# Kernel tuning notes

Hardware: AMD Instinct MI355X
Metric: run time of the kernel (lower is better)

Reference implementation:

```python
import jax, jax.numpy as jnp
import numpy as np

B, N, D = 32, 4096, 256
NC, NTPC, NVPT, NS = 16, 8, 4, 16
NT = NC * NTPC          # 128 type codes
NV = NT * NVPT          # 512 variant codes
THRESH = 0.1            # code_sparsity


def setup_inputs() -> dict:
    key = jax.random.key(0)
    ks = jax.random.split(key, 24)
    rn = lambda k, s, sc=0.02: jax.random.normal(k, s, jnp.float32) * sc
    return {
        "X": jax.random.normal(ks[0], (B, N, D), jnp.float32),
        "positions": jax.random.normal(ks[1], (B, N, D), jnp.float32),
        "mask": jnp.ones((B, N), jnp.bool_),
        "category_codes": rn(ks[2], (NC, D)),
        "type_codes": rn(ks[3], (NT, D)),
        "variant_codes": rn(ks[4], (NV, D)),
        "spatial_codes": rn(ks[5], (NS, D)),
        "log_tau": jnp.zeros((1,), jnp.float32),
        "Wk": rn(ks[6], (D, D)), "bk": jnp.zeros((D,), jnp.float32),
        "Wcat": rn(ks[7], (D, D)), "bcat": jnp.zeros((D,), jnp.float32),
        "Wtype": rn(ks[8], (D, D)), "btype": jnp.zeros((D,), jnp.float32),
        "Wvar": rn(ks[9], (D, D)), "bvar": jnp.zeros((D,), jnp.float32),
        "Wsp": rn(ks[10], (D, D)), "bsp": jnp.zeros((D,), jnp.float32),
        "Wg1": rn(ks[11], (D, 2 * D)), "bg1": jnp.zeros((D,), jnp.float32),
        "Wg2": rn(ks[12], (D, D)), "bg2": jnp.zeros((D,), jnp.float32),
        "Wo": rn(ks[13], (D, D)), "bo": jnp.zeros((D,), jnp.float32),
        "ln_g": jnp.ones((D,), jnp.float32), "ln_b": jnp.zeros((D,), jnp.float32),
        "level_weights": jnp.ones((4,), jnp.float32) / 4.0,
    }


def _sparsify(w, thr):
    w = jnp.where(w > thr, w, 0.0)
    return w / (w.sum(-1, keepdims=True) + 1e-8)


def reference(X, positions, mask, category_codes, type_codes, variant_codes,
              spatial_codes, log_tau, Wk, bk, Wcat, bcat, Wtype, btype,
              Wvar, bvar, Wsp, bsp, Wg1, bg1, Wg2, bg2, Wo, bo, ln_g, ln_b,
              level_weights):
    d = X.shape[-1]
    tau = jnp.clip(jnp.exp(log_tau) + 0.1, 0.1, 2.0)  # (1,)
    mv = jnp.finfo(X.dtype).min / 2
    K = X @ Wk.T + bk  # (B,N,d)

    def level(codes, Wq, bq):
        Q = codes @ Wq.T + bq                                    # (M,d)
        attn = jnp.einsum('md,bnd->bmn', Q, K) / jnp.sqrt(jnp.float32(d))
        attn = jnp.where(mask[:, None, :], attn, mv)
        attn = jnp.clip(attn, -50.0, 50.0)
        G = jnp.nan_to_num(jax.nn.softmax(attn, axis=-1))
        H = jnp.einsum('bmn,bnd->bmd', G, X)                     # (B,M,d)
        w_raw = jnp.linalg.norm(H, axis=-1) / tau                # (B,M)
        return H, w_raw

    # level 0: category
    H_cat, w_cat_raw = level(category_codes, Wcat, bcat)
    w_cat_sparse = _sparsify(jax.nn.softmax(w_cat_raw, -1), THRESH)
    # level 1: type (gated by category)
    H_type, w_type_raw = level(type_codes, Wtype, btype)
    w_type_g = (w_type_raw.reshape(-1, NC, NTPC) * w_cat_sparse[:, :, None]).reshape(-1, NT)
    w_type_sparse = _sparsify(jax.nn.softmax(w_type_g, -1), THRESH / 2)
    # level 2: variant (gated by type)
    H_var, w_var_raw = level(variant_codes, Wvar, bvar)
    w_type_exp = jnp.repeat(w_type_sparse, NVPT, axis=-1)        # (B,NV)
    w_var_sparse = _sparsify(jax.nn.softmax(w_var_raw * w_type_exp, -1), THRESH / 4)
    # spatial (independent)
    H_sp, w_sp_raw = level(spatial_codes, Wsp, bsp)
    w_sp_sparse = _sparsify(jax.nn.softmax(w_sp_raw, -1), THRESH)

    z_cat = jnp.einsum('bm,bmd->bd', w_cat_sparse, H_cat)
    z_type = jnp.einsum('bm,bmd->bd', w_type_sparse, H_type)
    z_var = jnp.einsum('bm,bmd->bd', w_var_sparse, H_var)
    z_sp = jnp.einsum('bm,bmd->bd', w_sp_sparse, H_sp)

    lw = jax.nn.softmax(level_weights)
    z = lw[0] * z_cat + lw[1] * z_type + lw[2] * z_var + lw[3] * z_sp

    # position gate: masked mean-pooled positions -> sigmoid gate
    m = mask.astype(X.dtype)
    pos_pool = (positions * m[:, :, None]).sum(1) / (m.sum(1, keepdims=True) + 1e-8)
    h = jax.nn.gelu(jnp.concatenate([z, pos_pool], -1) @ Wg1.T + bg1, approximate=False)
    gate = jax.nn.sigmoid(h @ Wg2.T + bg2)
    z = z * gate

    # out_proj: Linear + LayerNorm
    y = z @ Wo.T + bo
    mu = y.mean(-1, keepdims=True)
    var = ((y - mu) ** 2).mean(-1, keepdims=True)
    y = (y - mu) / jnp.sqrt(var + 1e-5) * ln_g + ln_b
    return y
```

## Files before the change

kernel.cpp:

```cpp
#include <hip/hip_runtime.h>

typedef unsigned short u16;
typedef short v8s __attribute__((ext_vector_type(8)));
typedef float v4f __attribute__((ext_vector_type(4)));

union U16x8 { uint4 u4; v8s s8; u16 us[8]; };

__device__ __forceinline__ u16 f2bf(float x) {
  unsigned int u = __float_as_uint(x);
  u += 0x7fffu + ((u >> 16) & 1u);
  return (u16)(u >> 16);
}

#define GLOBAL_AS __attribute__((address_space(1)))
#define LDS_AS __attribute__((address_space(3)))
__device__ __forceinline__ void async16(const void* g, void* l) {
  __builtin_amdgcn_global_load_lds((const GLOBAL_AS unsigned int*)g,
                                   (LDS_AS unsigned int*)l, 16, 0, 0);
}

#define BB 32
#define NN 4096
#define DD 256
#define M_TOT 672
#define M_PAD 704
#define MT_PER_B 11
#define NSPLIT 4
#define NCHUNK (NN / NSPLIT)

__global__ void k01_q(const float* __restrict__ cat, const float* __restrict__ typ,
                      const float* __restrict__ var, const float* __restrict__ spc,
                      const float* __restrict__ Wcat, const float* __restrict__ bcat,
                      const float* __restrict__ Wtype, const float* __restrict__ btype,
                      const float* __restrict__ Wvar, const float* __restrict__ bvar,
                      const float* __restrict__ Wsp, const float* __restrict__ bsp,
                      const float* __restrict__ Wk, const float* __restrict__ bk,
                      u16* __restrict__ Qp, float* __restrict__ qbw) {
  __shared__ float cl[DD];
  __shared__ float ql[DD];
  __shared__ float red[4];
  const int m = blockIdx.x, tid = threadIdx.x;
  const float* codes = nullptr; const float* W = nullptr; const float* bia = nullptr; int r = 0;
  if (m < 16)       { codes = cat; r = m;       W = Wcat;  bia = bcat; }
  else if (m < 144) { codes = typ; r = m - 16;  W = Wtype; bia = btype; }
  else if (m < 656) { codes = var; r = m - 144; W = Wvar;  bia = bvar; }
  else if (m < 672) { codes = spc; r = m - 656; W = Wsp;   bia = bsp; }
  cl[tid] = (m < M_TOT) ? codes[r * DD + tid] : 0.f;
  __syncthreads();
  float acc = 0.f;
  if (m < M_TOT) {
    acc = bia[tid];
    const float4* w4 = (const float4*)(W + (size_t)tid * DD);
    const float4* c4 = (const float4*)cl;
    #pragma unroll 8
    for (int k = 0; k < 64; ++k) {
      float4 a = c4[k], b = w4[k];
      acc += a.x * b.x + a.y * b.y + a.z * b.z + a.w * b.w;
    }
  }
  ql[tid] = acc;
  __syncthreads();
  float acc2 = 0.f;
  for (int j = 0; j < DD; ++j) acc2 += ql[j] * Wk[(size_t)j * DD + tid];
  Qp[m * DD + tid] = f2bf(acc2);
  float p = ql[tid] * bk[tid];
  #pragma unroll
  for (int off = 32; off > 0; off >>= 1) p += __shfl_down(p, off, 64);
  if ((tid & 63) == 0) red[tid >> 6] = p;
  __syncthreads();
  if (tid == 0) qbw[m] = red[0] + red[1] + red[2] + red[3];
}

__global__ void k2_cast(const float* __restrict__ X, u16* __restrict__ Xb,
                        u16* __restrict__ XbT) {
  __shared__ u16 tl[64][72];
  const int n0 = blockIdx.x * 64, d0 = blockIdx.y * 64, b = blockIdx.z;
  const int tid = threadIdx.x;
  const int nl = tid >> 4, d4 = tid & 15;
  #pragma unroll
  for (int rr = 0; rr < 4; ++rr) {
    const int n = n0 + nl + rr * 16;
    float4 v = *(const float4*)(X + ((size_t)b * NN + n) * DD + d0 + d4 * 4);
    ushort4 h;
    h.x = f2bf(v.x); h.y = f2bf(v.y); h.z = f2bf(v.z); h.w = f2bf(v.w);
    *(ushort4*)(Xb + ((size_t)b * NN + n) * DD + d0 +
                (((d4 >> 1) ^ (n & 7)) << 3) + (d4 & 1) * 4) = h;
    *(ushort4*)(&tl[nl + rr * 16][d4 * 4]) = h;
  }
  __syncthreads();
  const int dl = tid >> 4, n4 = tid & 15;
  #pragma unroll
  for (int rr = 0; rr < 4; ++rr) {
    const int d = dl + rr * 16;
    ushort4 h;
    h.x = tl[n4 * 4 + 0][d]; h.y = tl[n4 * 4 + 1][d];
    h.z = tl[n4 * 4 + 2][d]; h.w = tl[n4 * 4 + 3][d];
    *(ushort4*)(XbT + ((size_t)b * DD + d0 + d) * NN + n0 +
                (((n4 >> 1) ^ (dl & 7)) << 3) + (n4 & 1) * 4) = h;
  }
}

__global__ __launch_bounds__(256, 2) void pf_fused(
    const u16* __restrict__ Xb, const u16* __restrict__ XbT,
    const u16* __restrict__ Qp, const float* __restrict__ qbw,
    const unsigned char* __restrict__ mask,
    float* __restrict__ HP, float* __restrict__ sumsP) {
  __shared__ u16 sX[64 * 256];
  __shared__ u16 sXT[256 * 64];
  __shared__ u16 sP[64 * 64];

  const int id = blockIdx.x;
  const int xcd = id & 7, lin = id >> 3;
  const int ggl = lin / MT_PER_B, k = lin - ggl * MT_PER_B;
  const int gg = xcd * 16 + ggl;
  const int b = gg >> 2, split = gg & 3;
  const int m0 = k * 64;
  const int ns0 = split * NCHUNK;

  const int tid = threadIdx.x;
  const int lane = tid & 63, w = tid >> 6;
  const int q = lane >> 4, c16 = lane & 15;
  const int wmQ = (w >> 1) * 32, wn = (w & 1) * 32;
  const int wd = w * 64;

  const u16* XbB = Xb + (size_t)b * NN * DD;
  const u16* XTB = XbT + (size_t)b * DD * NN;
  const unsigned char* mkB = mask + (size_t)b * NN;

  auto stageX = [&](int n0g) {
    #pragma unroll
    for (int i = 0; i < 8; ++i) {
      const int c = i * 256 + tid;
      async16(XbB + (size_t)(n0g + (c >> 5)) * DD + (c & 31) * 8, sX + c * 8);
    }
  };
  auto stageT = [&](int n0g) {
    #pragma unroll
    for (int i = 0; i < 8; ++i) {
      const int c = i * 256 + tid;
      async16(XTB + (size_t)(c >> 3) * NN + n0g + (c & 7) * 8, sXT + c * 8);
    }
  };

  v8s aq[2][4][2];
  #pragma unroll
  for (int mi = 0; mi < 2; ++mi) {
    const u16* qrow = Qp + (size_t)(m0 + wmQ + mi * 16 + c16) * DD;
    #pragma unroll
    for (int ks = 0; ks < 4; ++ks)
      #pragma unroll
      for (int kk = 0; kk < 2; ++kk) {
        U16x8 u; u.u4 = *(const uint4*)(qrow + ks * 64 + kk * 32 + q * 8);
        aq[mi][ks][kk] = u.s8;
      }
  }
  float qv[2][4];
  #pragma unroll
  for (int mi = 0; mi < 2; ++mi)
    #pragma unroll
    for (int r = 0; r < 4; ++r)
      qv[mi][r] = qbw[m0 + wmQ + mi * 16 + q * 4 + r];

  v4f hacc[4][4];
  #pragma unroll
  for (int mi = 0; mi < 4; ++mi)
    #pragma unroll
    for (int di = 0; di < 4; ++di) hacc[mi][di] = (v4f){0.f, 0.f, 0.f, 0.f};
  float rs[2][4];
  #pragma unroll
  for (int mi = 0; mi < 2; ++mi)
    #pragma unroll
    for (int r = 0; r < 4; ++r) rs[mi][r] = 0.f;

  const int NT = NCHUNK / 64;
  stageX(ns0);
  stageT(ns0);
  __syncthreads();

  for (int it = 0; it < NT; ++it) {
    const int n0g = ns0 + it * 64;

    v4f sacc[2][2];
    #pragma unroll
    for (int mi = 0; mi < 2; ++mi)
      #pragma unroll
      for (int ni = 0; ni < 2; ++ni) sacc[mi][ni] = (v4f){0.f, 0.f, 0.f, 0.f};
    #pragma unroll
    for (int ks = 0; ks < 4; ++ks)
      #pragma unroll
      for (int kk = 0; kk < 2; ++kk) {
        v8s bq[2];
        #pragma unroll
        for (int ni = 0; ni < 2; ++ni) {
          const int n = wn + ni * 16 + c16;
          U16x8 u;
          u.u4 = *(const uint4*)(sX + n * 256 + (((ks * 8 + kk * 4 + q) ^ (n & 7)) << 3));
          bq[ni] = u.s8;
        }
        #pragma unroll
        for (int mi = 0; mi < 2; ++mi)
          #pragma unroll
          for (int ni = 0; ni < 2; ++ni)
            sacc[mi][ni] = __builtin_amdgcn_mfma_f32_16x16x32_bf16(
                aq[mi][ks][kk], bq[ni], sacc[mi][ni], 0, 0, 0);
      }

    #pragma unroll
    for (int ni = 0; ni < 2; ++ni) {
      const int nl = wn + ni * 16 + c16;
      const bool mk = mkB[n0g + nl] != 0;
      #pragma unroll
      for (int mi = 0; mi < 2; ++mi)
        #pragma unroll
        for (int r = 0; r < 4; ++r) {
          float s = (sacc[mi][ni][r] + qv[mi][r]) * 0.0625f;
          s = fminf(fmaxf(s, -50.f), 50.f);
          s = mk ? s : -50.f;
          float p = __expf(s);
          rs[mi][r] += p;
          const int ml = wmQ + mi * 16 + q * 4 + r;
          sP[ml * 64 + (nl ^ ((ml & 7) << 3))] = f2bf(p);
        }
    }
    __syncthreads();

    if (it + 1 < NT) stageX(n0g + 64);

    #pragma unroll
    for (int kk = 0; kk < 2; ++kk) {
      v8s pa[4];
      #pragma unroll
      for (int mi = 0; mi < 4; ++mi) {
        const int ml = mi * 16 + c16;
        U16x8 u;
        u.u4 = *(const uint4*)(sP + ml * 64 + ((kk * 32 + q * 8) ^ ((ml & 7) << 3)));
        pa[mi] = u.s8;
      }
      #pragma unroll
      for (int di = 0; di < 4; ++di) {
        const int d = wd + di * 16 + c16;
        U16x8 u;
        u.u4 = *(const uint4*)(sXT + d * 64 + (((kk * 4 + q) ^ (d & 7)) << 3));
        #pragma unroll
        for (int mi = 0; mi < 4; ++mi)
          hacc[mi][di] = __builtin_amdgcn_mfma_f32_16x16x32_bf16(
              pa[mi], u.s8, hacc[mi][di], 0, 0, 0);
      }
    }

    if (it + 1 < NT) {
      __syncthreads();
      stageT(n0g + 64);
    }
  }

  float* HPb = HP + ((size_t)split * BB + b) * M_PAD * DD;
  #pragma unroll
  for (int mi = 0; mi < 4; ++mi)
    #pragma unroll
    for (int di = 0; di < 4; ++di)
      #pragma unroll
      for (int r = 0; r < 4; ++r) {
        const int m = m0 + mi * 16 + q * 4 + r;
        HPb[(size_t)m * DD + wd + di * 16 + c16] = hacc[mi][di][r];
      }

  __syncthreads();
  float* fred = (float*)sP;
  #pragma unroll
  for (int mi = 0; mi < 2; ++mi)
    #pragma unroll
    for (int r = 0; r < 4; ++r) {
      float v = rs[mi][r];
      v += __shfl_xor(v, 1, 64);
      v += __shfl_xor(v, 2, 64);
      v += __shfl_xor(v, 4, 64);
      v += __shfl_xor(v, 8, 64);
      if (c16 == 0) fred[(w & 1) * 64 + wmQ + mi * 16 + q * 4 + r] = v;
    }
  __syncthreads();
  if (tid < 64) {
    sumsP[((size_t)split * BB + b) * M_PAD + m0 + tid] = fred[tid] + fred[64 + tid];
  }
}

__global__ void khr_reduce(float* __restrict__ HP, const float* __restrict__ sumsP,
                           float* __restrict__ sums, float* __restrict__ nrm) {
  __shared__ float red[64][4];
  const int mt = blockIdx.x, b = blockIdx.y, tid = threadIdx.x;
  const int lane = tid & 63, w = tid >> 6;
  const int m0 = mt * 64;
  const size_t SP = (size_t)BB * M_PAD * DD;
  float* base = HP + ((size_t)b * M_PAD + m0) * DD;
  for (int mi = 0; mi < 64; ++mi) {
    const size_t idx = (size_t)mi * DD + tid;
    float h = base[idx] + base[idx + SP] + base[idx + 2 * SP] + base[idx + 3 * SP];
    base[idx] = h;
    float v = h * h;
    v += __shfl_xor(v, 1, 64);
    v += __shfl_xor(v, 2, 64);
    v += __shfl_xor(v, 4, 64);
    v += __shfl_xor(v, 8, 64);
    v += __shfl_xor(v, 16, 64);
    v += __shfl_xor(v, 32, 64);
    if (lane == 0) red[mi][w] = v;
  }
  __syncthreads();
  if (tid < 64) {
    const size_t o = (size_t)b * M_PAD + m0 + tid;
    nrm[o] = red[tid][0] + red[tid][1] + red[tid][2] + red[tid][3];
    const size_t ss = (size_t)BB * M_PAD;
    const size_t si = (size_t)b * M_PAD + m0 + tid;
    sums[o] = sumsP[si] + sumsP[si + ss] + sumsP[si + 2 * ss] + sumsP[si + 3 * ss];
  }
}

__global__ void k4_pool(const float* __restrict__ pos, const unsigned char* __restrict__ mask,
                        float* __restrict__ pp, float* __restrict__ cnt) {
  __shared__ float sp[4][256];
  __shared__ float sc[4];
  const int cx = blockIdx.x, b = blockIdx.y, tid = threadIdx.x;
  const int nl = tid >> 6, d4 = tid & 63;
  const int n0 = cx * 256;
  float4 acc = {0.f, 0.f, 0.f, 0.f};
  float c = 0.f;
  for (int i = 0; i < 64; ++i) {
    const int n = n0 + i * 4 + nl;
    const float m = mask[(size_t)b * NN + n] ? 1.f : 0.f;
    c += m;
    float4 v = *(const float4*)(pos + ((size_t)b * NN + n) * DD + d4 * 4);
    acc.x += m * v.x; acc.y += m * v.y; acc.z += m * v.z; acc.w += m * v.w;
  }
  *(float4*)(&sp[nl][d4 * 4]) = acc;
  if (d4 == 0) sc[nl] = c;
  __syncthreads();
  pp[((size_t)b * 16 + cx) * DD + tid] = sp[0][tid] + sp[1][tid] + sp[2][tid] + sp[3][tid];
  if (tid == 0) cnt[b * 16 + cx] = sc[0] + sc[1] + sc[2] + sc[3];
}

__device__ void softmax_sparsify(const float* in, int nn, float* outp, float thr) {
  float mx = -3.4e38f;
  for (int i = 0; i < nn; ++i) mx = fmaxf(mx, in[i]);
  float s = 0.f;
  for (int i = 0; i < nn; ++i) { float e = __expf(in[i] - mx); outp[i] = e; s += e; }
  float s2 = 0.f;
  for (int i = 0; i < nn; ++i) {
    float v = outp[i] / s;
    v = (v > thr) ? v : 0.f;
    outp[i] = v; s2 += v;
  }
  const float inv = 1.f / (s2 + 1e-8f);
  for (int i = 0; i < nn; ++i) outp[i] *= inv;
}

__global__ void k5a_weights(const float* __restrict__ nrm, const float* __restrict__ sums,
                            const float* __restrict__ log_tau,
                            const float* __restrict__ lvlw, float* __restrict__ wbufG) {
  __shared__ float wr[M_TOT];
  __shared__ float wcat[16], wtyp[128], wvar[512], wsp[16], lw[4];
  __shared__ float tmp[128];
  const int b = blockIdx.x, tid = threadIdx.x;
  const float tau = fminf(fmaxf(__expf(log_tau[0]) + 0.1f, 0.1f), 2.0f);
  for (int m = tid; m < M_TOT; m += 256)
    wr[m] = sqrtf(nrm[(size_t)b * M_PAD + m]) / (sums[(size_t)b * M_PAD + m] * tau);
  __syncthreads();
  if (tid == 0) {
    softmax_sparsify(wr, 16, wcat, 0.1f);
    for (int i = 0; i < 128; ++i) tmp[i] = wr[16 + i] * wcat[i >> 3];
    softmax_sparsify(tmp, 128, wtyp, 0.05f);
    for (int i = 0; i < 512; ++i) wvar[i] = wr[144 + i] * wtyp[i >> 2];
    softmax_sparsify(wvar, 512, wvar, 0.025f);
    softmax_sparsify(wr + 656, 16, wsp, 0.1f);
    float mx = fmaxf(fmaxf(lvlw[0], lvlw[1]), fmaxf(lvlw[2], lvlw[3]));
    float s = 0.f;
    for (int i = 0; i < 4; ++i) { lw[i] = __expf(lvlw[i] - mx); s += lw[i]; }
    for (int i = 0; i < 4; ++i) lw[i] /= s;
  }
  __syncthreads();
  for (int m = tid; m < M_TOT; m += 256) {
    float v;
    if (m < 16)       v = lw[0] * wcat[m];
    else if (m < 144) v = lw[1] * wtyp[m - 16];
    else if (m < 656) v = lw[2] * wvar[m - 144];
    else              v = lw[3] * wsp[m - 656];
    wbufG[(size_t)b * M_PAD + m] = v / sums[(size_t)b * M_PAD + m];
  }
}

__global__ void k5b_z(const float* __restrict__ Hws, const float* __restrict__ wbufG,
                      float* __restrict__ zaccP) {
  const int mc = blockIdx.x, b = blockIdx.y, tid = threadIdx.x;
  const float* Hb = Hws + (size_t)b * M_PAD * DD;
  const float* wb = wbufG + (size_t)b * M_PAD;
  float acc = 0.f;
  #pragma unroll 4
  for (int i = 0; i < 84; ++i) {
    const int m = mc * 84 + i;
    acc += wb[m] * Hb[(size_t)m * DD + tid];
  }
  zaccP[((size_t)mc * BB + b) * DD + tid] = acc;
}

__global__ void k5c_mlp(const float* __restrict__ zaccP, const float* __restrict__ pp,
                        const float* __restrict__ cnt,
                        const float* __restrict__ Wg1, const float* __restrict__ bg1,
                        const float* __restrict__ Wg2, const float* __restrict__ bg2,
                        const float* __restrict__ Wo, const float* __restrict__ bo,
                        const float* __restrict__ lng, const float* __restrict__ lnb,
                        float* __restrict__ out) {
  __shared__ float zb[DD], pb[DD], hb[DD], zg[DD];
  __shared__ float red[8];
  const int b = blockIdx.x, tid = threadIdx.x;
  const int lane = tid & 63, w = tid >> 6;

  float p = 0.f, c = 0.f;
  for (int ch = 0; ch < 16; ++ch) {
    p += pp[((size_t)b * 16 + ch) * DD + tid];
    c += cnt[b * 16 + ch];
  }
  float z = 0.f;
  for (int ch = 0; ch < 8; ++ch)
    z += zaccP[((size_t)ch * BB + b) * DD + tid];
  zb[tid] = z;
  pb[tid] = p / (c + 1e-8f);
  __syncthreads();

  float h = bg1[tid];
  {
    const float4* w4 = (const float4*)(Wg1 + (size_t)tid * 512);
    const float4* z4 = (const float4*)zb;
    const float4* p4 = (const float4*)pb;
    for (int k = 0; k < 64; ++k) {
      float4 a = z4[k], bb = w4[k];
      h += a.x * bb.x + a.y * bb.y + a.z * bb.z + a.w * bb.w;
    }
    for (int k = 0; k < 64; ++k) {
      float4 a = p4[k], bb = w4[64 + k];
      h += a.x * bb.x + a.y * bb.y + a.z * bb.z + a.w * bb.w;
    }
  }
  h = 0.5f * h * (1.f + erff(h * 0.70710678118654752f));
  hb[tid] = h;
  __syncthreads();

  float g = bg2[tid];
  {
    const float4* w4 = (const float4*)(Wg2 + (size_t)tid * DD);
    const float4* h4 = (const float4*)hb;
    for (int k = 0; k < 64; ++k) {
      float4 a = h4[k], bb = w4[k];
      g += a.x * bb.x + a.y * bb.y + a.z * bb.z + a.w * bb.w;
    }
  }
  g = 1.f / (1.f + __expf(-g));
  zg[tid] = zb[tid] * g;
  __syncthreads();

  float y = bo[tid];
  {
    const float4* w4 = (const float4*)(Wo + (size_t)tid * DD);
    const float4* z4 = (const float4*)zg;
    for (int k = 0; k < 64; ++k) {
      float4 a = z4[k], bb = w4[k];
      y += a.x * bb.x + a.y * bb.y + a.z * bb.z + a.w * bb.w;
    }
  }

  float s = y;
  #pragma unroll
  for (int off = 32; off > 0; off >>= 1) s += __shfl_xor(s, off, 64);
  if (lane == 0) red[w] = s;
  __syncthreads();
  const float mu = (red[0] + red[1] + red[2] + red[3]) * (1.f / 256.f);
  float dv = (y - mu) * (y - mu);
  #pragma unroll
  for (int off = 32; off > 0; off >>= 1) dv += __shfl_xor(dv, off, 64);
  if (lane == 0) red[4 + w] = dv;
  __syncthreads();
  const float var = (red[4] + red[5] + red[6] + red[7]) * (1.f / 256.f);
  out[(size_t)b * DD + tid] = (y - mu) / sqrtf(var + 1e-5f) * lng[tid] + lnb[tid];
}

extern "C" void kernel_launch(void* const* d_in, const int* in_sizes, int n_in,
                              void* d_out, int out_size, void* d_ws, size_t ws_size,
                              hipStream_t stream) {
  const float* X          = (const float*)d_in[0];
  const float* positions  = (const float*)d_in[1];
  const unsigned char* mask = (const unsigned char*)d_in[2];
  const float* cat  = (const float*)d_in[3];
  const float* typ  = (const float*)d_in[4];
  const float* var  = (const float*)d_in[5];
  const float* spc  = (const float*)d_in[6];
  const float* log_tau = (const float*)d_in[7];
  const float* Wk   = (const float*)d_in[8];   const float* bk    = (const float*)d_in[9];
  const float* Wcat = (const float*)d_in[10];  const float* bcat  = (const float*)d_in[11];
  const float* Wtype= (const float*)d_in[12];  const float* btype = (const float*)d_in[13];
  const float* Wvar = (const float*)d_in[14];  const float* bvar  = (const float*)d_in[15];
  const float* Wsp  = (const float*)d_in[16];  const float* bsp   = (const float*)d_in[17];
  const float* Wg1  = (const float*)d_in[18];  const float* bg1   = (const float*)d_in[19];
  const float* Wg2  = (const float*)d_in[20];  const float* bg2   = (const float*)d_in[21];
  const float* Wo   = (const float*)d_in[22];  const float* bo    = (const float*)d_in[23];
  const float* lng  = (const float*)d_in[24];  const float* lnb   = (const float*)d_in[25];
  const float* lvlw = (const float*)d_in[26];

  char* ws = (char*)d_ws;
  size_t off = 0;
  auto alloc = [&](size_t bytes) { size_t o = off; off = (off + bytes + 255) & ~255ULL; return o; };
  const size_t oXb   = alloc((size_t)BB * NN * DD * 2);
  const size_t oXT   = alloc((size_t)BB * DD * NN * 2);
  const size_t oQp   = alloc((size_t)M_PAD * DD * 2);
  const size_t oQb   = alloc((size_t)M_PAD * 4);
  const size_t oSums = alloc((size_t)BB * M_PAD * 4);
  const size_t oSumsP= alloc((size_t)NSPLIT * BB * M_PAD * 4);
  const size_t oNrm  = alloc((size_t)BB * M_PAD * 4);
  const size_t oZacP = alloc((size_t)8 * BB * DD * 4);
  const size_t oWbf  = alloc((size_t)BB * M_PAD * 4);
  const size_t oHP   = alloc((size_t)NSPLIT * BB * M_PAD * DD * 4);
  const size_t oPP   = alloc((size_t)BB * 16 * DD * 4);
  const size_t oCNT  = alloc((size_t)BB * 16 * 4);

  u16*   Xb   = (u16*)(ws + oXb);
  u16*   XbT  = (u16*)(ws + oXT);
  u16*   Qp   = (u16*)(ws + oQp);
  float* qbw  = (float*)(ws + oQb);
  float* sums = (float*)(ws + oSums);
  float* sumsP= (float*)(ws + oSumsP);
  float* nrm  = (float*)(ws + oNrm);
  float* zaccP= (float*)(ws + oZacP);
  float* wbfG = (float*)(ws + oWbf);
  float* HP   = (float*)(ws + oHP);
  float* ppw  = (float*)(ws + oPP);
  float* cntw = (float*)(ws + oCNT);

  k01_q<<<M_PAD, 256, 0, stream>>>(cat, typ, var, spc, Wcat, bcat, Wtype, btype,
                                   Wvar, bvar, Wsp, bsp, Wk, bk, Qp, qbw);
  k2_cast<<<dim3(64, 4, 32), 256, 0, stream>>>(X, Xb, XbT);
  k4_pool<<<dim3(16, 32), 256, 0, stream>>>(positions, mask, ppw, cntw);
  pf_fused<<<dim3(BB * MT_PER_B * NSPLIT), 256, 0, stream>>>(Xb, XbT, Qp, qbw, mask,
                                                             HP, sumsP);
  khr_reduce<<<dim3(MT_PER_B, BB), 256, 0, stream>>>(HP, sumsP, sums, nrm);
  k5a_weights<<<32, 256, 0, stream>>>(nrm, sums, log_tau, lvlw, wbfG);
  k5b_z<<<dim3(8, 32), 256, 0, stream>>>(HP, wbfG, zaccP);
  k5c_mlp<<<32, 256, 0, stream>>>(zaccP, ppw, cntw, Wg1, bg1, Wg2, bg2, Wo, bo,
                                  lng, lnb, (float*)d_out);
}
```

Baseline: 705.8 us.

## Shrink attention tile to 32 columns for occupancy and fuse tail kernels

Halves the N tile in the fused attention kernel, re-swizzling the LDS layouts and padding the X rows, so LDS usage drops and three blocks per CU can be resident. The split-reduction, weight, z-accumulation and MLP kernels are merged into one per-batch kernel that re-reads the partial H buffers directly. This removes several launches and intermediate buffers, but the reduction over the large HP buffer now runs on only 32 blocks and reads it twice.

New measurement: 1.314 ms. +86.2%, slower.

```diff
diff --git a/kernel.cpp b/kernel.cpp
--- a/kernel.cpp
+++ b/kernel.cpp
@@ -27,6 +27,7 @@
 #define MT_PER_B 11
 #define NSPLIT 4
 #define NCHUNK (NN / NSPLIT)
+#define NBLK 32
 
 __global__ void k01_q(const float* __restrict__ cat, const float* __restrict__ typ,
                       const float* __restrict__ var, const float* __restrict__ spc,
@@ -95,19 +96,19 @@
     ushort4 h;
     h.x = tl[n4 * 4 + 0][d]; h.y = tl[n4 * 4 + 1][d];
     h.z = tl[n4 * 4 + 2][d]; h.w = tl[n4 * 4 + 3][d];
-    *(ushort4*)(XbT + ((size_t)b * DD + d0 + d) * NN + n0 +
-                (((n4 >> 1) ^ (dl & 7)) << 3) + (n4 & 1) * 4) = h;
-  }
-}
-
-__global__ __launch_bounds__(256, 2) void pf_fused(
+    *(ushort4*)(XbT + ((size_t)b * DD + d0 + d) * NN + n0 + (n4 >> 3) * 32 +
+                ((((n4 >> 1) & 3) ^ ((d >> 1) & 3)) << 3) + (n4 & 1) * 4) = h;
+  }
+}
+
+__global__ __launch_bounds__(256, 3) void pf_fused(
     const u16* __restrict__ Xb, const u16* __restrict__ XbT,
     const u16* __restrict__ Qp, const float* __restrict__ qbw,
     const unsigned char* __restrict__ mask,
     float* __restrict__ HP, float* __restrict__ sumsP) {
-  __shared__ u16 sX[64 * 256];
-  __shared__ u16 sXT[256 * 64];
-  __shared__ u16 sP[64 * 64];
+  __shared__ u16 sX[8448];
+  __shared__ u16 sXT[256 * 32];
+  __shared__ u16 sP[64 * 32];
 
   const int id = blockIdx.x;
   const int xcd = id & 7, lin = id >> 3;
@@ -120,7 +121,7 @@
   const int tid = threadIdx.x;
   const int lane = tid & 63, w = tid >> 6;
   const int q = lane >> 4, c16 = lane & 15;
-  const int wmQ = (w >> 1) * 32, wn = (w & 1) * 32;
+  const int wmQ = (w >> 1) * 32, wn = (w & 1) * 16;
   const int wd = w * 64;
 
   const u16* XbB = Xb + (size_t)b * NN * DD;
@@ -129,16 +130,17 @@
 
   auto stageX = [&](int n0g) {
     #pragma unroll
-    for (int i = 0; i < 8; ++i) {
+    for (int i = 0; i < 4; ++i) {
       const int c = i * 256 + tid;
-      async16(XbB + (size_t)(n0g + (c >> 5)) * DD + (c & 31) * 8, sX + c * 8);
+      async16(XbB + (size_t)(n0g + (c >> 5)) * DD + (c & 31) * 8,
+              sX + (c >> 6) * 528 + (c & 63) * 8);
     }
   };
   auto stageT = [&](int n0g) {
     #pragma unroll
-    for (int i = 0; i < 8; ++i) {
+    for (int i = 0; i < 4; ++i) {
       const int c = i * 256 + tid;
-      async16(XTB + (size_t)(c >> 3) * NN + n0g + (c & 7) * 8, sXT + c * 8);
+      async16(XTB + (size_t)(c >> 2) * NN + n0g + (c & 3) * 8, sXT + c * 8);
     }
   };
 
@@ -172,75 +174,67 @@
     #pragma unroll
     for (int r = 0; r < 4; ++r) rs[mi][r] = 0.f;
 
-  const int NT = NCHUNK / 64;
+  const int NT = NCHUNK / NBLK;
   stageX(ns0);
   stageT(ns0);
   __syncthreads();
 
+  const int nl = wn + c16;
+  const u16* sxrow = sX + (nl >> 1) * 528 + (nl & 1) * 256;
+  const int nx7 = nl & 7;
+
   for (int it = 0; it < NT; ++it) {
-    const int n0g = ns0 + it * 64;
-
-    v4f sacc[2][2];
-    #pragma unroll
-    for (int mi = 0; mi < 2; ++mi)
-      #pragma unroll
-      for (int ni = 0; ni < 2; ++ni) sacc[mi][ni] = (v4f){0.f, 0.f, 0.f, 0.f};
+    const int n0g = ns0 + it * NBLK;
+
+    v4f sacc[2];
+    sacc[0] = (v4f){0.f, 0.f, 0.f, 0.f};
+    sacc[1] = (v4f){0.f, 0.f, 0.f, 0.f};
     #pragma unroll
     for (int ks = 0; ks < 4; ++ks)
       #pragma unroll
       for (int kk = 0; kk < 2; ++kk) {
-        v8s bq[2];
-        #pragma unroll
-        for (int ni = 0; ni < 2; ++ni) {
-          const int n = wn + ni * 16 + c16;
-          U16x8 u;
-          u.u4 = *(const uint4*)(sX + n * 256 + (((ks * 8 + kk * 4 + q) ^ (n & 7)) << 3));
-          bq[ni] = u.s8;
-        }
+        U16x8 u;
+        u.u4 = *(const uint4*)(sxrow + (((ks * 8 + kk * 4 + q) ^ nx7) << 3));
         #pragma unroll
         for (int mi = 0; mi < 2; ++mi)
-          #pragma unroll
-          for (int ni = 0; ni < 2; ++ni)
-            sacc[mi][ni] = __builtin_amdgcn_mfma_f32_16x16x32_bf16(
-                aq[mi][ks][kk], bq[ni], sacc[mi][ni], 0, 0, 0);
+          sacc[mi] = __builtin_amdgcn_mfma_f32_16x16x32_bf16(
+              aq[mi][ks][kk], u.s8, sacc[mi], 0, 0, 0);
       }
 
-    #pragma unroll
-    for (int ni = 0; ni < 2; ++ni) {
-      const int nl = wn + ni * 16 + c16;
+    {
       const bool mk = mkB[n0g + nl] != 0;
       #pragma unroll
       for (int mi = 0; mi < 2; ++mi)
         #pragma unroll
         for (int r = 0; r < 4; ++r) {
-          float s = (sacc[mi][ni][r] + qv[mi][r]) * 0.0625f;
+          float s = (sacc[mi][r] + qv[mi][r]) * 0.0625f;
           s = fminf(fmaxf(s, -50.f), 50.f);
           s = mk ? s : -50.f;
           float p = __expf(s);
           rs[mi][r] += p;
           const int ml = wmQ + mi * 16 + q * 4 + r;
-          sP[ml * 64 + (nl ^ ((ml & 7) << 3))] = f2bf(p);
+          sP[ml * 32 + (nl ^ (((ml & 3) ^ ((ml >> 2) & 3)) << 3))] = f2bf(p);
         }
     }
     __syncthreads();
 
-    if (it + 1 < NT) stageX(n0g + 64);
-
-    #pragma unroll
-    for (int kk = 0; kk < 2; ++kk) {
+    if (it + 1 < NT) stageX(n0g + NBLK);
+
+    {
       v8s pa[4];
       #pragma unroll
       for (int mi = 0; mi < 4; ++mi) {
-        const int ml = mi * 16 + c16;
+        const int ml2 = mi * 16 + c16;
         U16x8 u;
-        u.u4 = *(const uint4*)(sP + ml * 64 + ((kk * 32 + q * 8) ^ ((ml & 7) << 3)));
+        u.u4 = *(const uint4*)(sP + ml2 * 32 +
+                               ((q * 8) ^ ((((ml2 & 3) ^ ((ml2 >> 2) & 3)) << 3))));
         pa[mi] = u.s8;
       }
       #pragma unroll
       for (int di = 0; di < 4; ++di) {
         const int d = wd + di * 16 + c16;
         U16x8 u;
-        u.u4 = *(const uint4*)(sXT + d * 64 + (((kk * 4 + q) ^ (d & 7)) << 3));
+        u.u4 = *(const uint4*)(sXT + d * 32 + ((q ^ ((d >> 1) & 3)) << 3));
         #pragma unroll
         for (int mi = 0; mi < 4; ++mi)
           hacc[mi][di] = __builtin_amdgcn_mfma_f32_16x16x32_bf16(
@@ -250,7 +244,7 @@
 
     if (it + 1 < NT) {
       __syncthreads();
-      stageT(n0g + 64);
+      stageT(n0g + NBLK);
     }
   }
 
@@ -281,37 +275,6 @@
   __syncthreads();
   if (tid < 64) {
     sumsP[((size_t)split * BB + b) * M_PAD + m0 + tid] = fred[tid] + fred[64 + tid];
-  }
-}
-
-__global__ void khr_reduce(float* __restrict__ HP, const float* __restrict__ sumsP,
-                           float* __restrict__ sums, float* __restrict__ nrm) {
-  __shared__ float red[64][4];
-  const int mt = blockIdx.x, b = blockIdx.y, tid = threadIdx.x;
-  const int lane = tid & 63, w = tid >> 6;
-  const int m0 = mt * 64;
-  const size_t SP = (size_t)BB * M_PAD * DD;
-  float* base = HP + ((size_t)b * M_PAD + m0) * DD;
-  for (int mi = 0; mi < 64; ++mi) {
-    const size_t idx = (size_t)mi * DD + tid;
-    float h = base[idx] + base[idx + SP] + base[idx + 2 * SP] + base[idx + 3 * SP];
-    base[idx] = h;
-    float v = h * h;
-    v += __shfl_xor(v, 1, 64);
-    v += __shfl_xor(v, 2, 64);
-    v += __shfl_xor(v, 4, 64);
-    v += __shfl_xor(v, 8, 64);
-    v += __shfl_xor(v, 16, 64);
-    v += __shfl_xor(v, 32, 64);
-    if (lane == 0) red[mi][w] = v;
-  }
-  __syncthreads();
-  if (tid < 64) {
-    const size_t o = (size_t)b * M_PAD + m0 + tid;
-    nrm[o] = red[tid][0] + red[tid][1] + red[tid][2] + red[tid][3];
-    const size_t ss = (size_t)BB * M_PAD;
-    const size_t si = (size_t)b * M_PAD + m0 + tid;
-    sums[o] = sumsP[si] + sumsP[si + ss] + sumsP[si + 2 * ss] + sumsP[si + 3 * ss];
   }
 }
 
@@ -353,23 +316,54 @@
   for (int i = 0; i < nn; ++i) outp[i] *= inv;
 }
 
-__global__ void k5a_weights(const float* __restrict__ nrm, const float* __restrict__ sums,
-                            const float* __restrict__ log_tau,
-                            const float* __restrict__ lvlw, float* __restrict__ wbufG) {
-  __shared__ float wr[M_TOT];
-  __shared__ float wcat[16], wtyp[128], wvar[512], wsp[16], lw[4];
-  __shared__ float tmp[128];
+__global__ void k5f(const float* __restrict__ HP, const float* __restrict__ sumsP,
+                    const float* __restrict__ pp, const float* __restrict__ cnt,
+                    const float* __restrict__ log_tau, const float* __restrict__ lvlw,
+                    const float* __restrict__ Wg1, const float* __restrict__ bg1,
+                    const float* __restrict__ Wg2, const float* __restrict__ bg2,
+                    const float* __restrict__ Wo, const float* __restrict__ bo,
+                    const float* __restrict__ lng, const float* __restrict__ lnb,
+                    float* __restrict__ out) {
+  __shared__ float wpart[M_TOT * 4];
+  __shared__ float wr[M_TOT], sar[M_TOT], wbuf[M_TOT];
+  __shared__ float wcat[16], wtyp[128], wvarS[512], wsp[16], lw[4], tmp[128];
+  __shared__ float zb[DD], pb[DD], hb[DD], zg[DD];
+  __shared__ float red[8];
   const int b = blockIdx.x, tid = threadIdx.x;
+  const int lane = tid & 63, w = tid >> 6;
+  const size_t SP = (size_t)BB * M_PAD * DD;
+  const size_t SS = (size_t)BB * M_PAD;
+  const float* H0 = HP + (size_t)b * M_PAD * DD;
+
+  for (int m = 0; m < M_TOT; ++m) {
+    const float* r0 = H0 + (size_t)m * DD + tid;
+    float h = r0[0] + r0[SP] + r0[2 * SP] + r0[3 * SP];
+    float v = h * h;
+    v += __shfl_xor(v, 1, 64);
+    v += __shfl_xor(v, 2, 64);
+    v += __shfl_xor(v, 4, 64);
+    v += __shfl_xor(v, 8, 64);
+    v += __shfl_xor(v, 16, 64);
+    v += __shfl_xor(v, 32, 64);
+    if (lane == 0) wpart[m * 4 + w] = v;
+  }
+  __syncthreads();
   const float tau = fminf(fmaxf(__expf(log_tau[0]) + 0.1f, 0.1f), 2.0f);
-  for (int m = tid; m < M_TOT; m += 256)
-    wr[m] = sqrtf(nrm[(size_t)b * M_PAD + m]) / (sums[(size_t)b * M_PAD + m] * tau);
-  __syncthreads();
+  for (int m = tid; m < M_TOT; m += 256) {
+    float nr = wpart[m * 4] + wpart[m * 4 + 1] + wpart[m * 4 + 2] + wpart[m * 4 + 3];
+    const size_t si = (size_t)b * M_PAD + m;
+    float sm = sumsP[si] + sumsP[si + SS] + sumsP[si + 2 * SS] + sumsP[si + 3 * SS];
+    wr[m] = sqrtf(nr) / (sm * tau);
+    sar[m] = sm;
+  }
+  __syncthreads();
+
   if (tid == 0) {
     softmax_sparsify(wr, 16, wcat, 0.1f);
     for (int i = 0; i < 128; ++i) tmp[i] = wr[16 + i] * wcat[i >> 3];
     softmax_sparsify(tmp, 128, wtyp, 0.05f);
-    for (int i = 0; i < 512; ++i) wvar[i] = wr[144 + i] * wtyp[i >> 2];
-    softmax_sparsify(wvar, 512, wvar, 0.025f);
+    for (int i = 0; i < 512; ++i) wvarS[i] = wr[144 + i] * wtyp[i >> 2];
+    softmax_sparsify(wvarS, 512, wvarS, 0.025f);
     softmax_sparsify(wr + 656, 16, wsp, 0.1f);
     float mx = fmaxf(fmaxf(lvlw[0], lvlw[1]), fmaxf(lvlw[2], lvlw[3]));
     float s = 0.f;
@@ -381,46 +375,26 @@
     float v;
     if (m < 16)       v = lw[0] * wcat[m];
     else if (m < 144) v = lw[1] * wtyp[m - 16];
-    else if (m < 656) v = lw[2] * wvar[m - 144];
+    else if (m < 656) v = lw[2] * wvarS[m - 144];
     else              v = lw[3] * wsp[m - 656];
-    wbufG[(size_t)b * M_PAD + m] = v / sums[(size_t)b * M_PAD + m];
-  }
-}
-
-__global__ void k5b_z(const float* __restrict__ Hws, const float* __restrict__ wbufG,
-                      float* __restrict__ zaccP) {
-  const int mc = blockIdx.x, b = blockIdx.y, tid = threadIdx.x;
-  const float* Hb = Hws + (size_t)b * M_PAD * DD;
-  const float* wb = wbufG + (size_t)b * M_PAD;
-  float acc = 0.f;
-  #pragma unroll 4
-  for (int i = 0; i < 84; ++i) {
-    const int m = mc * 84 + i;
-    acc += wb[m] * Hb[(size_t)m * DD + tid];
-  }
-  zaccP[((size_t)mc * BB + b) * DD + tid] = acc;
-}
-
-__global__ void k5c_mlp(const float* __restrict__ zaccP, const float* __restrict__ pp,
-                        const float* __restrict__ cnt,
-                        const float* __restrict__ Wg1, const float* __restrict__ bg1,
-                        const float* __restrict__ Wg2, const float* __restrict__ bg2,
-                        const float* __restrict__ Wo, const float* __restrict__ bo,
-                        const float* __restrict__ lng, const float* __restrict__ lnb,
-                        float* __restrict__ out) {
-  __shared__ float zb[DD], pb[DD], hb[DD], zg[DD];
-  __shared__ float red[8];
-  const int b = blockIdx.x, tid = threadIdx.x;
-  const int lane = tid & 63, w = tid >> 6;
+    wbuf[m] = v / sar[m];
+  }
+  __syncthreads();
+
+  float z = 0.f;
+  for (int m = 0; m < M_TOT; m += 2) {
+    const float* ra = H0 + (size_t)m * DD + tid;
+    const float* rb = ra + DD;
+    float ha = ra[0] + ra[SP] + ra[2 * SP] + ra[3 * SP];
+    float hc = rb[0] + rb[SP] + rb[2 * SP] + rb[3 * SP];
+    z += wbuf[m] * ha + wbuf[m + 1] * hc;
+  }
 
   float p = 0.f, c = 0.f;
   for (int ch = 0; ch < 16; ++ch) {
     p += pp[((size_t)b * 16 + ch) * DD + tid];
     c += cnt[b * 16 + ch];
   }
-  float z = 0.f;
-  for (int ch = 0; ch < 8; ++ch)
-    z += zaccP[((size_t)ch * BB + b) * DD + tid];
   zb[tid] = z;
   pb[tid] = p / (c + 1e-8f);
   __syncthreads();
@@ -510,11 +484,7 @@
   const size_t oXT   = alloc((size_t)BB * DD * NN * 2);
   const size_t oQp   = alloc((size_t)M_PAD * DD * 2);
   const size_t oQb   = alloc((size_t)M_PAD * 4);
-  const size_t oSums = alloc((size_t)BB * M_PAD * 4);
   const size_t oSumsP= alloc((size_t)NSPLIT * BB * M_PAD * 4);
-  const size_t oNrm  = alloc((size_t)BB * M_PAD * 4);
-  const size_t oZacP = alloc((size_t)8 * BB * DD * 4);
-  const size_t oWbf  = alloc((size_t)BB * M_PAD * 4);
   const size_t oHP   = alloc((size_t)NSPLIT * BB * M_PAD * DD * 4);
   const size_t oPP   = alloc((size_t)BB * 16 * DD * 4);
   const size_t oCNT  = alloc((size_t)BB * 16 * 4);
@@ -523,11 +493,7 @@
   u16*   XbT  = (u16*)(ws + oXT);
   u16*   Qp   = (u16*)(ws + oQp);
   float* qbw  = (float*)(ws + oQb);
-  float* sums = (float*)(ws + oSums);
   float* sumsP= (float*)(ws + oSumsP);
-  float* nrm  = (float*)(ws + oNrm);
-  float* zaccP= (float*)(ws + oZacP);
-  float* wbfG = (float*)(ws + oWbf);
   float* HP   = (float*)(ws + oHP);
   float* ppw  = (float*)(ws + oPP);
   float* cntw = (float*)(ws + oCNT);
@@ -538,9 +504,6 @@
   k4_pool<<<dim3(16, 32), 256, 0, stream>>>(positions, mask, ppw, cntw);
   pf_fused<<<dim3(BB * MT_PER_B * NSPLIT), 256, 0, stream>>>(Xb, XbT, Qp, qbw, mask,
                                                              HP, sumsP);
-  khr_reduce<<<dim3(MT_PER_B, BB), 256, 0, stream>>>(HP, sumsP, sums, nrm);
-  k5a_weights<<<32, 256, 0, stream>>>(nrm, sums, log_tau, lvlw, wbfG);
-  k5b_z<<<dim3(8, 32), 256, 0, stream>>>(HP, wbfG, zaccP);
-  k5c_mlp<<<32, 256, 0, stream>>>(zaccP, ppw, cntw, Wg1, bg1, Wg2, bg2, Wo, bo,
-                                  lng, lnb, (float*)d_out);
-}
+  k5f<<<32, 256, 0, stream>>>(HP, sumsP, ppw, cntw, log_tau, lvlw,
+                              Wg1, bg1, Wg2, bg2, Wo, bo, lng, lnb, (float*)d_out);
+}
```
